# Kernel tuning notes

Hardware: AMD Instinct MI355X
Metric: run time of the kernel (lower is better)

The kernel has to match this reference:

```python
import jax, jax.numpy as jnp
import numpy as np

N_NODES = 25000
N_EDGES = 400000
IN_DIM = 64
HID = 64
EMB = 8
N_GRAPHS = 16
N_CLASSES = 10
BN_EPS = 1e-5
NORM_EPS = 1e-12


def setup_inputs() -> dict:
    key = jax.random.key(0)
    ks = jax.random.split(key, 20)
    inp = {
        "feature": jax.random.normal(ks[0], (N_NODES, IN_DIM), jnp.float32),
        "sp_embeddings": jax.random.normal(ks[1], (N_NODES, EMB), jnp.float32),
        "src": jax.random.randint(ks[2], (N_EDGES,), 0, N_NODES, jnp.int32),
        "dst": jax.random.randint(ks[3], (N_EDGES,), 0, N_NODES, jnp.int32),
        "graph_ids": jnp.sort(jax.random.randint(ks[4], (N_NODES,), 0, N_GRAPHS, jnp.int32)),
        # per-layer bilinear weights (embeddim, in, out), xavier-ish scale
        "W0": jax.random.normal(ks[5], (EMB, IN_DIM, HID), jnp.float32) * (2.0 / (IN_DIM + HID)) ** 0.5,
        "W1": jax.random.normal(ks[6], (EMB, HID, HID), jnp.float32) * (1.0 / HID) ** 0.5,
        "W2": jax.random.normal(ks[7], (EMB, HID, HID), jnp.float32) * (1.0 / HID) ** 0.5,
        "g0": jnp.ones((HID,), jnp.float32), "b0": jnp.zeros((HID,), jnp.float32),
        "g1": jnp.ones((HID,), jnp.float32), "b1": jnp.zeros((HID,), jnp.float32),
        "g2": jnp.ones((HID,), jnp.float32), "b2": jnp.zeros((HID,), jnp.float32),
        # classifier MLP: hidden -> hidden/2 (BN+ReLU) -> num_classes
        "cW1": jax.random.normal(ks[8], (HID, HID // 2), jnp.float32) * (1.0 / HID) ** 0.5,
        "cb1": jnp.zeros((HID // 2,), jnp.float32),
        "cg1": jnp.ones((HID // 2,), jnp.float32),
        "cbt1": jnp.zeros((HID // 2,), jnp.float32),
        "cW2": jax.random.normal(ks[9], (HID // 2, N_CLASSES), jnp.float32) * (2.0 / HID) ** 0.5,
        "cb2": jnp.zeros((N_CLASSES,), jnp.float32),
    }
    return inp


def _batchnorm(x, gamma, beta):
    # training-mode BatchNorm1d: biased batch statistics over dim 0
    mu = jnp.mean(x, axis=0)
    var = jnp.mean((x - mu) ** 2, axis=0)
    return gamma * (x - mu) * jax.lax.rsqrt(var + BN_EPS) + beta


def _gconv_layer(h, c, src, dst, W, gamma, beta, shortcut):
    # direction = L2-normalize(c[src] - c[dst])  (F.normalize eps=1e-12)
    d = c[src] - c[dst]                                   # [E, EMB]
    nrm = jnp.sqrt(jnp.sum(d * d, axis=1, keepdims=True))
    d = d / jnp.maximum(nrm, NORM_EPS)
    # per-edge bilinear: einsum('ei,ijk,ej->ek')
    msg = jnp.einsum('ei,ijk,ej->ek', d, W, h[src])        # [E, out]
    agg = jax.ops.segment_sum(msg, dst, num_segments=N_NODES)
    out = _batchnorm(jax.nn.relu(agg), gamma, beta)
    if shortcut:
        out = out + h
    return out


def _classifier(x, cW1, cb1, cg1, cbt1, cW2, cb2):
    h1 = jax.nn.relu(_batchnorm(x @ cW1 + cb1, cg1, cbt1))
    return h1 @ cW2 + cb2


def reference(feature, sp_embeddings, src, dst, graph_ids,
              W0, W1, W2, g0, b0, g1, b1, g2, b2,
              cW1, cb1, cg1, cbt1, cW2, cb2):
    h = feature
    logits = jnp.zeros((N_GRAPHS, N_CLASSES), jnp.float32)
    layer_params = [(W0, g0, b0, False), (W1, g1, b1, True), (W2, g2, b2, True)]
    for W, g, b, sc in layer_params:
        h = _gconv_layer(h, sp_embeddings, src, dst, W, g, b, sc)
        pooled = jax.ops.segment_sum(h, graph_ids, num_segments=N_GRAPHS)
        # dropout treated as identity (eval mode)
        logits = logits + _classifier(pooled, cW1, cb1, cg1, cbt1, cW2, cb2)
    return logits
```

## Files before the change

### kernel.cpp

```cpp
#include <hip/hip_runtime.h>
#include <hip/hip_fp16.h>
#include <math.h>

#define NN 25000
#define NE 400000
#define HD 64
#define EMBD 8
#define NG 16
#define NC 10
#define SCAN_NB 98
#define NSL 16
#define STATS_F (NSL * 64 + NSL * 64 + NSL * 1024)

typedef _Float16 f16x8 __attribute__((ext_vector_type(8)));
typedef float f32x4 __attribute__((ext_vector_type(4)));

__global__ __launch_bounds__(256) void hist_k(const int* __restrict__ dst, int* cnt) {
    int e = blockIdx.x * 256 + threadIdx.x;
    if (e < NE) atomicAdd(&cnt[dst[e]], 1);
}

__global__ __launch_bounds__(256) void scan_part_k(const int* __restrict__ cnt, int* bsum) {
    __shared__ int sh[256];
    int tx = threadIdx.x;
    int i = blockIdx.x * 256 + tx;
    sh[tx] = (i < NN) ? cnt[i] : 0;
    __syncthreads();
    for (int off = 128; off > 0; off >>= 1) {
        if (tx < off) sh[tx] += sh[tx + off];
        __syncthreads();
    }
    if (tx == 0) bsum[blockIdx.x] = sh[0];
}

__global__ __launch_bounds__(128) void scan_mid_k(const int* __restrict__ bsum,
        int* boff, int* dstoff, const int* __restrict__ gids, int* gcnt) {
    __shared__ int sh[128];
    int tx = threadIdx.x;
    int v = (tx < SCAN_NB) ? bsum[tx] : 0;
    sh[tx] = v;
    __syncthreads();
    for (int off = 1; off < 128; off <<= 1) {
        int t = (tx >= off) ? sh[tx - off] : 0;
        __syncthreads();
        sh[tx] += t;
        __syncthreads();
    }
    if (tx < SCAN_NB) boff[tx] = sh[tx] - v;
    if (tx == 0) dstoff[NN] = NE;
    if (tx < NG) {
        int lo = 0, hi = NN;
        while (lo < hi) { int m = (lo + hi) >> 1; if (gids[m] < tx) lo = m + 1; else hi = m; }
        int a = lo;
        lo = 0; hi = NN;
        while (lo < hi) { int m = (lo + hi) >> 1; if (gids[m] < tx + 1) lo = m + 1; else hi = m; }
        gcnt[tx] = lo - a;
    }
}

__global__ __launch_bounds__(256) void scan_final_k(const int* __restrict__ cnt,
        const int* __restrict__ boff, int* dstoff, int* cur) {
    __shared__ int sh[256];
    int tx = threadIdx.x;
    int i = blockIdx.x * 256 + tx;
    int v = (i < NN) ? cnt[i] : 0;
    sh[tx] = v;
    __syncthreads();
    for (int off = 1; off < 256; off <<= 1) {
        int t = (tx >= off) ? sh[tx - off] : 0;
        __syncthreads();
        sh[tx] += t;
        __syncthreads();
    }
    int excl = boff[blockIdx.x] + sh[tx] - v;
    if (i < NN) { dstoff[i] = excl; cur[i] = excl; }
}

__global__ __launch_bounds__(256) void prep_k(const int* __restrict__ src,
        const int* __restrict__ dst, const float* __restrict__ c,
        int* cur, int* __restrict__ src_d, float* __restrict__ dnorm_d,
        const float* __restrict__ feature, __half* __restrict__ h16,
        const float* __restrict__ W0, const float* __restrict__ W1,
        const float* __restrict__ W2, __half* __restrict__ Wt,
        float* __restrict__ statsAll) {
    int gid = blockIdx.x * 256 + threadIdx.x;

    if (gid < NE) {
        int s = src[gid], t = dst[gid];
        int pd = atomicAdd(&cur[t], 1);
        src_d[pd] = s;
        float4 sa = *(const float4*)(c + (size_t)s * 8);
        float4 sb = *(const float4*)(c + (size_t)s * 8 + 4);
        float4 na = *(const float4*)(c + (size_t)t * 8);
        float4 nb = *(const float4*)(c + (size_t)t * 8 + 4);
        float d0 = sa.x - na.x, d1 = sa.y - na.y, d2 = sa.z - na.z, d3 = sa.w - na.w;
        float d4 = sb.x - nb.x, d5 = sb.y - nb.y, d6 = sb.z - nb.z, d7 = sb.w - nb.w;
        float nn2 = d0*d0 + d1*d1 + d2*d2 + d3*d3 + d4*d4 + d5*d5 + d6*d6 + d7*d7;
        float inv = 1.f / fmaxf(sqrtf(nn2), 1e-12f);
        *(float4*)(dnorm_d + (size_t)pd * 8)     = make_float4(d0*inv, d1*inv, d2*inv, d3*inv);
        *(float4*)(dnorm_d + (size_t)pd * 8 + 4) = make_float4(d4*inv, d5*inv, d6*inv, d7*inv);
    }
    if (gid < NN * 16) {
        float4 v = *(const float4*)(feature + (size_t)gid * 4);
        __half2 lo = __floats2half2_rn(v.x, v.y);
        __half2 hi = __floats2half2_rn(v.z, v.w);
        *(__half2*)(h16 + (size_t)gid * 4)     = lo;
        *(__half2*)(h16 + (size_t)gid * 4 + 2) = hi;
    }
    if (gid < 3 * STATS_F) statsAll[gid] = 0.f;
    if (gid < 3 * 64 * 512) {
        int l = gid >> 15;
        int rem = gid & 32767;
        int k = rem >> 9;
        int qp = rem & 511;
        int ii = qp & 7;
        int jj = qp >> 3;
        const float* W = (l == 0) ? W0 : ((l == 1) ? W1 : W2);
        Wt[gid] = __float2half_rn(W[(size_t)(ii * 64 + jj) * 64 + k]);
    }
}

__global__ __launch_bounds__(256) void edge_gemm_k(const int* __restrict__ src_d,
        const int* __restrict__ dstoff, const float* __restrict__ dnorm_d,
        const __half* __restrict__ h16, const __half* __restrict__ Wt16,
        const int* __restrict__ gids, float* __restrict__ agg,
        float* __restrict__ sumsN, float* __restrict__ sumsqN,
        float* __restrict__ XgN) {
    __shared__ __half Esh[16][520];
    __shared__ float pl[NG * 64];
    __shared__ float s1[64], s2[64];
    __shared__ int gsh[16];
    int tx = threadIdx.x;
    int wave = tx >> 6, lane = tx & 63;
    int n0 = blockIdx.x * 16;
    int slice = blockIdx.x & (NSL - 1);
    for (int t = tx; t < NG * 64; t += 256) pl[t] = 0.f;
    if (tx < 64) { s1[tx] = 0.f; s2[tx] = 0.f; }
    if (tx < 16) gsh[tx] = gids[min(n0 + tx, NN - 1)];

#pragma unroll
    for (int i = 0; i < 4; i++) {
        int nloc = wave * 4 + i;
        int n = n0 + nloc;
        float e0=0,e1=0,e2=0,e3=0,e4=0,e5=0,e6=0,e7=0;
        if (n < NN) {
            int p0 = dstoff[n], p1 = dstoff[n + 1];
            for (int p = p0; p < p1; p += 8) {
                int m = p1 - p;
                int pj[8]; int sj[8]; __half hj[8];
#pragma unroll
                for (int j = 0; j < 8; j++) {
                    int q = p + j; if (q > p1 - 1) q = p1 - 1;
                    pj[j] = q;
                    sj[j] = src_d[q];
                }
#pragma unroll
                for (int j = 0; j < 8; j++)
                    hj[j] = h16[(size_t)sj[j] * 64 + lane];
#pragma unroll
                for (int j = 0; j < 8; j++)
                    if (j < m) {
                        float4 dA = *(const float4*)(dnorm_d + (size_t)pj[j] * 8);
                        float4 dB = *(const float4*)(dnorm_d + (size_t)pj[j] * 8 + 4);
                        float hv = __half2float(hj[j]);
                        e0 = fmaf(dA.x, hv, e0); e1 = fmaf(dA.y, hv, e1);
                        e2 = fmaf(dA.z, hv, e2); e3 = fmaf(dA.w, hv, e3);
                        e4 = fmaf(dB.x, hv, e4); e5 = fmaf(dB.y, hv, e5);
                        e6 = fmaf(dB.z, hv, e6); e7 = fmaf(dB.w, hv, e7);
                    }
            }
        }
        float4 pack;
        ((__half2*)&pack)[0] = __floats2half2_rn(e0, e1);
        ((__half2*)&pack)[1] = __floats2half2_rn(e2, e3);
        ((__half2*)&pack)[2] = __floats2half2_rn(e4, e5);
        ((__half2*)&pack)[3] = __floats2half2_rn(e6, e7);
        *(float4*)&Esh[nloc][lane * 8] = pack;
    }
    __syncthreads();

    int quad = lane >> 4;
    int lcol = lane & 15;
    int c0 = wave * 16;
    const f16x8* pb = (const f16x8*)(Wt16 + (size_t)(c0 + lcol) * 512 + quad * 8);
    f32x4 acc = {0.f, 0.f, 0.f, 0.f};
#pragma unroll
    for (int kc = 0; kc < 16; kc++) {
        f16x8 a = *(const f16x8*)&Esh[lcol][kc * 32 + quad * 8];
        f16x8 b = pb[kc * 4];
        acc = __builtin_amdgcn_mfma_f32_16x16x32_f16(a, b, acc, 0, 0, 0);
    }

    int colg = c0 + lcol;
    float s1l = 0.f, s2l = 0.f;
#pragma unroll
    for (int r = 0; r < 4; r++) {
        int nrow = quad * 4 + r;
        int n = n0 + nrow;
        if (n < NN) {
            float v = acc[r];
            agg[(size_t)n * 64 + colg] = v;
            float x = fmaxf(v, 0.f);
            s1l += x; s2l += x * x;
            atomicAdd(&pl[gsh[nrow] * 64 + colg], x);
        }
    }
    atomicAdd(&s1[colg], s1l);
    atomicAdd(&s2[colg], s2l);
    __syncthreads();
    if (tx < 64) {
        atomicAdd(&sumsN[slice * 64 + tx], s1[tx]);
        atomicAdd(&sumsqN[slice * 64 + tx], s2[tx]);
    }
    for (int t = tx; t < NG * 64; t += 256) {
        float v = pl[t];
        if (v != 0.f) atomicAdd(&XgN[slice * 1024 + t], v);
    }
}

__device__ __forceinline__ void classifier_body(int tx,
        const float* __restrict__ sumsN, const float* __restrict__ sumsqN,
        const float* __restrict__ XgN, const int* __restrict__ gcnt,
        float* __restrict__ Pold,
        const float* __restrict__ gamma, const float* __restrict__ beta,
        const float* __restrict__ cW1, const float* __restrict__ cb1,
        const float* __restrict__ cg1, const float* __restrict__ cbt1,
        const float* __restrict__ cW2, const float* __restrict__ cb2,
        float* __restrict__ logits, int sc) {
    __shared__ float Pn[NG * 64];
    __shared__ float H1s[NG * 32];
    __shared__ float cmu[32], crs[32];
    for (int t = tx; t < NG * 64; t += 256) {
        int g = t >> 6, k = t & 63;
        float sk = 0.f, sq = 0.f, xg = 0.f;
#pragma unroll
        for (int s = 0; s < NSL; s++) {
            sk += sumsN[s * 64 + k];
            sq += sumsqN[s * 64 + k];
            xg += XgN[s * 1024 + t];
        }
        float mean = sk * (1.f / NN);
        float var  = sq * (1.f / NN) - mean * mean;
        float r = rsqrtf(var + 1e-5f);
        float cg = (float)gcnt[g];
        float v = gamma[k] * r * (xg - cg * mean) + cg * beta[k];
        if (sc) v += Pold[t];
        Pn[t] = v;
        Pold[t] = v;
    }
    __syncthreads();
    for (int t = tx; t < NG * 32; t += 256) {
        int g = t >> 5, c = t & 31;
        float acc = cb1[c];
#pragma unroll 16
        for (int j = 0; j < 64; j++) acc = fmaf(Pn[g * 64 + j], cW1[j * 32 + c], acc);
        H1s[t] = acc;
    }
    __syncthreads();
    if (tx < 32) {
        float mu = 0.f;
#pragma unroll
        for (int g2 = 0; g2 < NG; g2++) mu += H1s[g2 * 32 + tx];
        mu *= (1.f / NG);
        float v = 0.f;
#pragma unroll
        for (int g2 = 0; g2 < NG; g2++) {
            float d = H1s[g2 * 32 + tx] - mu;
            v += d * d;
        }
        v *= (1.f / NG);
        cmu[tx] = mu;
        crs[tx] = rsqrtf(v + 1e-5f);
    }
    __syncthreads();
    for (int t = tx; t < NG * 32; t += 256) {
        int c = t & 31;
        H1s[t] = fmaxf(cg1[c] * (H1s[t] - cmu[c]) * crs[c] + cbt1[c], 0.f);
    }
    __syncthreads();
    if (tx < NG * NC) {
        int g = tx / NC, cls = tx % NC;
        float a2 = cb2[cls];
#pragma unroll
        for (int j = 0; j < 32; j++) a2 = fmaf(H1s[g * 32 + j], cW2[j * NC + cls], a2);
        logits[tx] += a2;
    }
}

__global__ __launch_bounds__(256) void bn_apply_k(const float* __restrict__ agg,
        const float* __restrict__ h_old, const float* __restrict__ sumsN,
        const float* __restrict__ sumsqN, const float* __restrict__ gamma,
        const float* __restrict__ beta, float* __restrict__ h_new,
        __half* __restrict__ h16_out, int shortcut,
        const float* __restrict__ XgN, const int* __restrict__ gcnt,
        float* __restrict__ Pold,
        const float* __restrict__ cW1, const float* __restrict__ cb1,
        const float* __restrict__ cg1, const float* __restrict__ cbt1,
        const float* __restrict__ cW2, const float* __restrict__ cb2,
        float* __restrict__ logits) {
    int tx = threadIdx.x;
    int col0 = (tx & 15) * 4;
    float mean[4], rstd[4], gv[4], bv[4];
#pragma unroll
    for (int cc = 0; cc < 4; cc++) {
        int k = col0 + cc;
        float sk = 0.f, sq = 0.f;
#pragma unroll
        for (int s = 0; s < NSL; s++) {
            sk += sumsN[s * 64 + k];
            sq += sumsqN[s * 64 + k];
        }
        float mu = sk * (1.f / NN);
        float var = sq * (1.f / NN) - mu * mu;
        mean[cc] = mu;
        rstd[cc] = rsqrtf(var + 1e-5f);
        gv[cc] = gamma[k];
        bv[cc] = beta[k];
    }
    int row = blockIdx.x * 16 + (tx >> 4);
    int rstride = gridDim.x * 16;
    for (int n = row; n < NN; n += rstride) {
        float4 x4 = *(const float4*)(agg + (size_t)n * 64 + col0);
        float y[4] = {x4.x, x4.y, x4.z, x4.w};
#pragma unroll
        for (int cc = 0; cc < 4; cc++) {
            float x = fmaxf(y[cc], 0.f);
            y[cc] = gv[cc] * (x - mean[cc]) * rstd[cc] + bv[cc];
        }
        if (shortcut) {
            float4 h4 = *(const float4*)(h_old + (size_t)n * 64 + col0);
            y[0] += h4.x; y[1] += h4.y; y[2] += h4.z; y[3] += h4.w;
        }
        *(float4*)(h_new + (size_t)n * 64 + col0) = make_float4(y[0], y[1], y[2], y[3]);
        float2 pk;
        ((__half2*)&pk)[0] = __floats2half2_rn(y[0], y[1]);
        ((__half2*)&pk)[1] = __floats2half2_rn(y[2], y[3]);
        *(float2*)(h16_out + (size_t)n * 64 + col0) = pk;
    }
    if (blockIdx.x == 0)
        classifier_body(tx, sumsN, sumsqN, XgN, gcnt, Pold, gamma, beta,
                        cW1, cb1, cg1, cbt1, cW2, cb2, logits, shortcut);
}

__global__ __launch_bounds__(256) void classifier_only_k(
        const float* __restrict__ sumsN, const float* __restrict__ sumsqN,
        const float* __restrict__ XgN, const int* __restrict__ gcnt,
        float* __restrict__ Pold,
        const float* __restrict__ gamma, const float* __restrict__ beta,
        const float* __restrict__ cW1, const float* __restrict__ cb1,
        const float* __restrict__ cg1, const float* __restrict__ cbt1,
        const float* __restrict__ cW2, const float* __restrict__ cb2,
        float* __restrict__ logits) {
    classifier_body(threadIdx.x, sumsN, sumsqN, XgN, gcnt, Pold, gamma, beta,
                    cW1, cb1, cg1, cbt1, cW2, cb2, logits, 1);
}

extern "C" void kernel_launch(void* const* d_in, const int* in_sizes, int n_in,
                              void* d_out, int out_size, void* d_ws, size_t ws_size,
                              hipStream_t stream) {
    const float* feature = (const float*)d_in[0];
    const float* cemb    = (const float*)d_in[1];
    const int*   src     = (const int*)d_in[2];
    const int*   dst     = (const int*)d_in[3];
    const int*   gids    = (const int*)d_in[4];
    const float* W[3]    = {(const float*)d_in[5], (const float*)d_in[6], (const float*)d_in[7]};
    const float* gam[3]  = {(const float*)d_in[8], (const float*)d_in[10], (const float*)d_in[12]};
    const float* bet[3]  = {(const float*)d_in[9], (const float*)d_in[11], (const float*)d_in[13]};
    const float* cW1  = (const float*)d_in[14];
    const float* cb1  = (const float*)d_in[15];
    const float* cg1  = (const float*)d_in[16];
    const float* cbt1 = (const float*)d_in[17];
    const float* cW2  = (const float*)d_in[18];
    const float* cb2  = (const float*)d_in[19];
    float* out = (float*)d_out;

    float* ws       = (float*)d_ws;
    float* dnorm_d  = ws;
    float* bufX     = dnorm_d + (size_t)NE * 8;
    float* bufY     = bufX + (size_t)NN * 64;
    float* statsAll = bufY + (size_t)NN * 64;
    float* Pold     = statsAll + 3 * STATS_F;
    int*   cnt      = (int*)(Pold + 1024);
    int*   gcnt     = cnt + NN;
    int*   cur      = gcnt + 16;
    int*   dstoff   = cur + NN;
    int*   bsum     = dstoff + NN + 8;
    int*   boff     = bsum + 128;
    int*   src_d    = boff + 128;
    __half* h16     = (__half*)(src_d + NE);
    __half* Wt16    = (__half*)((float*)(src_d + NE) + (size_t)NN * 32);

    hipMemsetAsync(d_out, 0, (size_t)NG * NC * sizeof(float), stream);
    hipMemsetAsync(cnt, 0, NN * sizeof(int), stream);

    hist_k<<<(NE + 255) / 256, 256, 0, stream>>>(dst, cnt);
    scan_part_k<<<SCAN_NB, 256, 0, stream>>>(cnt, bsum);
    scan_mid_k<<<1, 128, 0, stream>>>(bsum, boff, dstoff, gids, gcnt);
    scan_final_k<<<SCAN_NB, 256, 0, stream>>>(cnt, boff, dstoff, cur);
    prep_k<<<(NE + 255) / 256, 256, 0, stream>>>(src, dst, cemb, cur, src_d, dnorm_d,
                                                 feature, h16, W[0], W[1], W[2], Wt16,
                                                 statsAll);

    const float* h_old = feature;
    float* bufs[2] = {bufX, bufY};
    for (int l = 0; l < 3; l++) {
        float* agg    = bufs[l & 1];
        float* sumsN  = statsAll + (size_t)l * STATS_F;
        float* sumsqN = sumsN + NSL * 64;
        float* XgN    = sumsqN + NSL * 64;

        edge_gemm_k<<<(NN + 15) / 16, 256, 0, stream>>>(src_d, dstoff, dnorm_d, h16,
                                                        Wt16 + (size_t)l * 64 * 512,
                                                        gids, agg, sumsN, sumsqN, XgN);
        if (l < 2) {
            bn_apply_k<<<1024, 256, 0, stream>>>(agg, h_old, sumsN, sumsqN, gam[l], bet[l],
                                                 agg, h16, l > 0, XgN, gcnt, Pold,
                                                 cW1, cb1, cg1, cbt1, cW2, cb2, out);
        } else {
            classifier_only_k<<<1, 256, 0, stream>>>(sumsN, sumsqN, XgN, gcnt, Pold,
                                                     gam[l], bet[l],
                                                     cW1, cb1, cg1, cbt1, cW2, cb2, out);
        }
        h_old = agg;
    }
}
```

Measured before the change: 366.7 us.

## Halve nodes per block and interleave two nodes' edge gathers per wave

After: 447.4 us. 1.22x slower.

```diff
diff --git a/kernel.cpp b/kernel.cpp
--- a/kernel.cpp
+++ b/kernel.cpp
@@ -129,65 +129,101 @@
     __shared__ __half Esh[16][520];
     __shared__ float pl[NG * 64];
     __shared__ float s1[64], s2[64];
-    __shared__ int gsh[16];
+    __shared__ int gsh[8];
     int tx = threadIdx.x;
     int wave = tx >> 6, lane = tx & 63;
-    int n0 = blockIdx.x * 16;
+    int n0 = blockIdx.x * 8;
     int slice = blockIdx.x & (NSL - 1);
     for (int t = tx; t < NG * 64; t += 256) pl[t] = 0.f;
     if (tx < 64) { s1[tx] = 0.f; s2[tx] = 0.f; }
-    if (tx < 16) gsh[tx] = gids[min(n0 + tx, NN - 1)];
-
-#pragma unroll
-    for (int i = 0; i < 4; i++) {
-        int nloc = wave * 4 + i;
-        int n = n0 + nloc;
-        float e0=0,e1=0,e2=0,e3=0,e4=0,e5=0,e6=0,e7=0;
-        if (n < NN) {
-            int p0 = dstoff[n], p1 = dstoff[n + 1];
-            for (int p = p0; p < p1; p += 8) {
-                int m = p1 - p;
-                int pj[8]; int sj[8]; __half hj[8];
-#pragma unroll
-                for (int j = 0; j < 8; j++) {
-                    int q = p + j; if (q > p1 - 1) q = p1 - 1;
-                    pj[j] = q;
-                    sj[j] = src_d[q];
-                }
-#pragma unroll
-                for (int j = 0; j < 8; j++)
-                    hj[j] = h16[(size_t)sj[j] * 64 + lane];
-#pragma unroll
-                for (int j = 0; j < 8; j++)
-                    if (j < m) {
-                        float4 dA = *(const float4*)(dnorm_d + (size_t)pj[j] * 8);
-                        float4 dB = *(const float4*)(dnorm_d + (size_t)pj[j] * 8 + 4);
-                        float hv = __half2float(hj[j]);
-                        e0 = fmaf(dA.x, hv, e0); e1 = fmaf(dA.y, hv, e1);
-                        e2 = fmaf(dA.z, hv, e2); e3 = fmaf(dA.w, hv, e3);
-                        e4 = fmaf(dB.x, hv, e4); e5 = fmaf(dB.y, hv, e5);
-                        e6 = fmaf(dB.z, hv, e6); e7 = fmaf(dB.w, hv, e7);
-                    }
+    if (tx < 8) gsh[tx] = gids[n0 + tx];
+    {
+        float4 z = make_float4(0.f, 0.f, 0.f, 0.f);
+        float4* zb = (float4*)&Esh[8][0];
+        for (int t = tx; t < 520; t += 256) zb[t] = z;
+    }
+
+    int nA = n0 + (wave << 1);
+    int a0 = dstoff[nA];
+    int a1 = dstoff[nA + 1];
+    int b1 = dstoff[nA + 2];
+    float eA[8] = {0,0,0,0,0,0,0,0};
+    float eB[8] = {0,0,0,0,0,0,0,0};
+    int pa = a0, pb = a1;
+    while (pa < a1 || pb < b1) {
+        bool doA = pa < a1, doB = pb < b1;
+        int sA[8], sB[8];
+        __half hA[8], hB[8];
+        if (doA) {
+#pragma unroll
+            for (int j = 0; j < 8; j++) sA[j] = src_d[min(pa + j, a1 - 1)];
+        }
+        if (doB) {
+#pragma unroll
+            for (int j = 0; j < 8; j++) sB[j] = src_d[min(pb + j, b1 - 1)];
+        }
+        if (doA) {
+#pragma unroll
+            for (int j = 0; j < 8; j++) hA[j] = h16[(size_t)sA[j] * 64 + lane];
+        }
+        if (doB) {
+#pragma unroll
+            for (int j = 0; j < 8; j++) hB[j] = h16[(size_t)sB[j] * 64 + lane];
+        }
+        if (doA) {
+#pragma unroll
+            for (int j = 0; j < 8; j++) {
+                int q = min(pa + j, a1 - 1);
+                float hv = (pa + j < a1) ? __half2float(hA[j]) : 0.f;
+                const float* dp = dnorm_d + (size_t)q * 8;
+                float4 d0 = *(const float4*)dp;
+                float4 d1 = *(const float4*)(dp + 4);
+                eA[0] = fmaf(d0.x, hv, eA[0]); eA[1] = fmaf(d0.y, hv, eA[1]);
+                eA[2] = fmaf(d0.z, hv, eA[2]); eA[3] = fmaf(d0.w, hv, eA[3]);
+                eA[4] = fmaf(d1.x, hv, eA[4]); eA[5] = fmaf(d1.y, hv, eA[5]);
+                eA[6] = fmaf(d1.z, hv, eA[6]); eA[7] = fmaf(d1.w, hv, eA[7]);
             }
         }
+        if (doB) {
+#pragma unroll
+            for (int j = 0; j < 8; j++) {
+                int q = min(pb + j, b1 - 1);
+                float hv = (pb + j < b1) ? __half2float(hB[j]) : 0.f;
+                const float* dp = dnorm_d + (size_t)q * 8;
+                float4 d0 = *(const float4*)dp;
+                float4 d1 = *(const float4*)(dp + 4);
+                eB[0] = fmaf(d0.x, hv, eB[0]); eB[1] = fmaf(d0.y, hv, eB[1]);
+                eB[2] = fmaf(d0.z, hv, eB[2]); eB[3] = fmaf(d0.w, hv, eB[3]);
+                eB[4] = fmaf(d1.x, hv, eB[4]); eB[5] = fmaf(d1.y, hv, eB[5]);
+                eB[6] = fmaf(d1.z, hv, eB[6]); eB[7] = fmaf(d1.w, hv, eB[7]);
+            }
+        }
+        pa += 8; pb += 8;
+    }
+    {
         float4 pack;
-        ((__half2*)&pack)[0] = __floats2half2_rn(e0, e1);
-        ((__half2*)&pack)[1] = __floats2half2_rn(e2, e3);
-        ((__half2*)&pack)[2] = __floats2half2_rn(e4, e5);
-        ((__half2*)&pack)[3] = __floats2half2_rn(e6, e7);
-        *(float4*)&Esh[nloc][lane * 8] = pack;
+        ((__half2*)&pack)[0] = __floats2half2_rn(eA[0], eA[1]);
+        ((__half2*)&pack)[1] = __floats2half2_rn(eA[2], eA[3]);
+        ((__half2*)&pack)[2] = __floats2half2_rn(eA[4], eA[5]);
+        ((__half2*)&pack)[3] = __floats2half2_rn(eA[6], eA[7]);
+        *(float4*)&Esh[wave * 2][lane * 8] = pack;
+        ((__half2*)&pack)[0] = __floats2half2_rn(eB[0], eB[1]);
+        ((__half2*)&pack)[1] = __floats2half2_rn(eB[2], eB[3]);
+        ((__half2*)&pack)[2] = __floats2half2_rn(eB[4], eB[5]);
+        ((__half2*)&pack)[3] = __floats2half2_rn(eB[6], eB[7]);
+        *(float4*)&Esh[wave * 2 + 1][lane * 8] = pack;
     }
     __syncthreads();
 
     int quad = lane >> 4;
     int lcol = lane & 15;
     int c0 = wave * 16;
-    const f16x8* pb = (const f16x8*)(Wt16 + (size_t)(c0 + lcol) * 512 + quad * 8);
+    const f16x8* pb16 = (const f16x8*)(Wt16 + (size_t)(c0 + lcol) * 512 + quad * 8);
     f32x4 acc = {0.f, 0.f, 0.f, 0.f};
 #pragma unroll
     for (int kc = 0; kc < 16; kc++) {
         f16x8 a = *(const f16x8*)&Esh[lcol][kc * 32 + quad * 8];
-        f16x8 b = pb[kc * 4];
+        f16x8 b = pb16[kc * 4];
         acc = __builtin_amdgcn_mfma_f32_16x16x32_f16(a, b, acc, 0, 0, 0);
     }
 
@@ -196,8 +232,8 @@
 #pragma unroll
     for (int r = 0; r < 4; r++) {
         int nrow = quad * 4 + r;
-        int n = n0 + nrow;
-        if (n < NN) {
+        if (nrow < 8) {
+            int n = n0 + nrow;
             float v = acc[r];
             agg[(size_t)n * 64 + colg] = v;
             float x = fmaxf(v, 0.f);
@@ -409,9 +445,9 @@
         float* sumsqN = sumsN + NSL * 64;
         float* XgN    = sumsqN + NSL * 64;
 
-        edge_gemm_k<<<(NN + 15) / 16, 256, 0, stream>>>(src_d, dstoff, dnorm_d, h16,
-                                                        Wt16 + (size_t)l * 64 * 512,
-                                                        gids, agg, sumsN, sumsqN, XgN);
+        edge_gemm_k<<<(NN + 7) / 8, 256, 0, stream>>>(src_d, dstoff, dnorm_d, h16,
+                                                      Wt16 + (size_t)l * 64 * 512,
+                                                      gids, agg, sumsN, sumsqN, XgN);
         if (l < 2) {
             bn_apply_k<<<1024, 256, 0, stream>>>(agg, h_old, sumsN, sumsqN, gam[l], bet[l],
                                                  agg, h16, l > 0, XgN, gcnt, Pold,
```

## Load edge metadata per lane and broadcast via readlane with double-buffered gathers

Applied to the files above, without the earlier changes.

After: 312.6 us. 14.8% less time.

```diff
diff --git a/kernel.cpp b/kernel.cpp
--- a/kernel.cpp
+++ b/kernel.cpp
@@ -120,7 +120,11 @@
     }
 }
 
-__global__ __launch_bounds__(256) void edge_gemm_k(const int* __restrict__ src_d,
+__device__ __forceinline__ float rlane(float v, int l) {
+    return __uint_as_float((unsigned)__builtin_amdgcn_readlane((int)__float_as_uint(v), l));
+}
+
+__global__ __launch_bounds__(256, 4) void edge_gemm_k(const int* __restrict__ src_d,
         const int* __restrict__ dstoff, const float* __restrict__ dnorm_d,
         const __half* __restrict__ h16, const __half* __restrict__ Wt16,
         const int* __restrict__ gids, float* __restrict__ agg,
@@ -134,40 +138,61 @@
     int wave = tx >> 6, lane = tx & 63;
     int n0 = blockIdx.x * 16;
     int slice = blockIdx.x & (NSL - 1);
+    const unsigned short* h16u = (const unsigned short*)h16;
     for (int t = tx; t < NG * 64; t += 256) pl[t] = 0.f;
     if (tx < 64) { s1[tx] = 0.f; s2[tx] = 0.f; }
     if (tx < 16) gsh[tx] = gids[min(n0 + tx, NN - 1)];
 
-#pragma unroll
+#define LOADG(dst, g) do { _Pragma("unroll") \
+    for (int j_ = 0; j_ < 8; j_++) { \
+        int s_ = __builtin_amdgcn_readlane(sv, (g) * 8 + j_); \
+        dst[j_] = (int)h16u[(size_t)s_ * 64 + lane]; \
+    } } while (0)
+
+#define FMAG(srcv, g) do { _Pragma("unroll") \
+    for (int j_ = 0; j_ < 8; j_++) { \
+        int jj_ = (g) * 8 + j_; \
+        __half hh_; *(unsigned short*)&hh_ = (unsigned short)srcv[j_]; \
+        float hv_ = (jj_ < rem) ? __half2float(hh_) : 0.f; \
+        e0 = fmaf(rlane(da.x, jj_), hv_, e0); \
+        e1 = fmaf(rlane(da.y, jj_), hv_, e1); \
+        e2 = fmaf(rlane(da.z, jj_), hv_, e2); \
+        e3 = fmaf(rlane(da.w, jj_), hv_, e3); \
+        e4 = fmaf(rlane(db.x, jj_), hv_, e4); \
+        e5 = fmaf(rlane(db.y, jj_), hv_, e5); \
+        e6 = fmaf(rlane(db.z, jj_), hv_, e6); \
+        e7 = fmaf(rlane(db.w, jj_), hv_, e7); \
+    } } while (0)
+
     for (int i = 0; i < 4; i++) {
         int nloc = wave * 4 + i;
         int n = n0 + nloc;
         float e0=0,e1=0,e2=0,e3=0,e4=0,e5=0,e6=0,e7=0;
         if (n < NN) {
             int p0 = dstoff[n], p1 = dstoff[n + 1];
-            for (int p = p0; p < p1; p += 8) {
-                int m = p1 - p;
-                int pj[8]; int sj[8]; __half hj[8];
-#pragma unroll
-                for (int j = 0; j < 8; j++) {
-                    int q = p + j; if (q > p1 - 1) q = p1 - 1;
-                    pj[j] = q;
-                    sj[j] = src_d[q];
-                }
-#pragma unroll
-                for (int j = 0; j < 8; j++)
-                    hj[j] = h16[(size_t)sj[j] * 64 + lane];
-#pragma unroll
-                for (int j = 0; j < 8; j++)
-                    if (j < m) {
-                        float4 dA = *(const float4*)(dnorm_d + (size_t)pj[j] * 8);
-                        float4 dB = *(const float4*)(dnorm_d + (size_t)pj[j] * 8 + 4);
-                        float hv = __half2float(hj[j]);
-                        e0 = fmaf(dA.x, hv, e0); e1 = fmaf(dA.y, hv, e1);
-                        e2 = fmaf(dA.z, hv, e2); e3 = fmaf(dA.w, hv, e3);
-                        e4 = fmaf(dB.x, hv, e4); e5 = fmaf(dB.y, hv, e5);
-                        e6 = fmaf(dB.z, hv, e6); e7 = fmaf(dB.w, hv, e7);
-                    }
+            for (int base = p0; base < p1; base += 64) {
+                int rem = p1 - base;
+                int eidx = min(base + lane, p1 - 1);
+                int sv = src_d[eidx];
+                float4 da = *(const float4*)(dnorm_d + (size_t)eidx * 8);
+                float4 db = *(const float4*)(dnorm_d + (size_t)eidx * 8 + 4);
+                int hA[8], hB[8];
+                LOADG(hA, 0);
+                if (rem > 8)  LOADG(hB, 1);
+                FMAG(hA, 0);
+                if (rem > 16) LOADG(hA, 2);
+                if (rem > 8)  FMAG(hB, 1);
+                if (rem > 24) LOADG(hB, 3);
+                if (rem > 16) FMAG(hA, 2);
+                if (rem > 32) LOADG(hA, 4);
+                if (rem > 24) FMAG(hB, 3);
+                if (rem > 40) LOADG(hB, 5);
+                if (rem > 32) FMAG(hA, 4);
+                if (rem > 48) LOADG(hA, 6);
+                if (rem > 40) FMAG(hB, 5);
+                if (rem > 56) LOADG(hB, 7);
+                if (rem > 48) FMAG(hA, 6);
+                if (rem > 56) FMAG(hB, 7);
             }
         }
         float4 pack;
@@ -177,6 +202,8 @@
         ((__half2*)&pack)[3] = __floats2half2_rn(e6, e7);
         *(float4*)&Esh[nloc][lane * 8] = pack;
     }
+#undef LOADG
+#undef FMAG
     __syncthreads();
 
     int quad = lane >> 4;
```
